# Performance work log

Measured on AMD Instinct MI355X. Metric: run time of the kernel, lower is better.

Reference implementation:

```python
import jax, jax.numpy as jnp
import numpy as np

N_PFAS, N_GW, N_SW = 20000, 100000, 30000
D, OUT = 128, 128
E_PG, E_GP, E_PS, E_SP = 1600000, 640000, 480000, 320000


def setup_inputs() -> dict:
    key = jax.random.key(0)
    ks = jax.random.split(key, 32)
    g = lambda k, shape, fan_in: jax.random.normal(k, shape, jnp.float32) / np.sqrt(fan_in)
    inp = {
        "x_pfas": jax.random.normal(ks[0], (N_PFAS, D), jnp.float32),
        "x_gw": jax.random.normal(ks[1], (N_GW, D), jnp.float32),
        "x_sw": jax.random.normal(ks[2], (N_SW, D), jnp.float32),
        "ei_pg_src": jax.random.randint(ks[3], (E_PG,), 0, N_PFAS),
        "ei_pg_dst": jax.random.randint(ks[4], (E_PG,), 0, N_GW),
        "ei_gp_src": jax.random.randint(ks[5], (E_GP,), 0, N_GW),
        "ei_gp_dst": jax.random.randint(ks[6], (E_GP,), 0, N_PFAS),
        "ei_ps_src": jax.random.randint(ks[7], (E_PS,), 0, N_PFAS),
        "ei_ps_dst": jax.random.randint(ks[8], (E_PS,), 0, N_SW),
        "ei_sp_src": jax.random.randint(ks[9], (E_SP,), 0, N_SW),
        "ei_sp_dst": jax.random.randint(ks[10], (E_SP,), 0, N_PFAS),
    }
    # SAGEConv params per relation: lin_l (on aggregated neighbors, with bias), lin_r (root, no bias)
    names = ["pg", "gp", "ps", "sp"]
    for i, n in enumerate(names):
        inp[f"Wl_{n}"] = g(ks[11 + 3 * i], (D, OUT), D)
        inp[f"bl_{n}"] = jnp.zeros((OUT,), jnp.float32)
        inp[f"Wr_{n}"] = g(ks[12 + 3 * i], (D, OUT), D)
    inp["W_gw"] = g(ks[25], (OUT, 1), OUT)
    inp["b_gw"] = jnp.zeros((1,), jnp.float32)
    inp["W_sw"] = g(ks[26], (OUT, 1), OUT)
    inp["b_sw"] = jnp.zeros((1,), jnp.float32)
    return inp


def _sage(x_src, x_dst, src, dst, n_dst, Wl, bl, Wr):
    # SAGEConv: lin_l(mean_j x_src[j]) + lin_r(x_dst)
    msg = x_src[src]  # [E, D] gather
    s = jax.ops.segment_sum(msg, dst, num_segments=n_dst)
    cnt = jax.ops.segment_sum(jnp.ones((src.shape[0],), x_src.dtype), dst, num_segments=n_dst)
    mean = s / jnp.maximum(cnt, 1.0)[:, None]
    return mean @ Wl + bl + x_dst @ Wr


def reference(x_pfas, x_gw, x_sw,
              ei_pg_src, ei_pg_dst, ei_gp_src, ei_gp_dst,
              ei_ps_src, ei_ps_dst, ei_sp_src, ei_sp_dst,
              Wl_pg, bl_pg, Wr_pg, Wl_gp, bl_gp, Wr_gp,
              Wl_ps, bl_ps, Wr_ps, Wl_sp, bl_sp, Wr_sp,
              W_gw, b_gw, W_sw, b_sw):
    h_gw = _sage(x_pfas, x_gw, ei_pg_src, ei_pg_dst, N_GW, Wl_pg, bl_pg, Wr_pg)
    h_sw = _sage(x_pfas, x_sw, ei_ps_src, ei_ps_dst, N_SW, Wl_ps, bl_ps, Wr_ps)
    # pfas_sites is the destination of two relations -> HeteroConv aggr='sum'
    h_pf = (_sage(x_gw, x_pfas, ei_gp_src, ei_gp_dst, N_PFAS, Wl_gp, bl_gp, Wr_gp)
            + _sage(x_sw, x_pfas, ei_sp_src, ei_sp_dst, N_PFAS, Wl_sp, bl_sp, Wr_sp))
    h_pf = jax.nn.relu(h_pf)
    h_gw = jax.nn.relu(h_gw)
    h_sw = jax.nn.relu(h_sw)
    out_gw = h_gw @ W_gw + b_gw   # [N_GW, 1]
    out_sw = h_sw @ W_sw + b_sw   # [N_SW, 1]
    return h_pf, out_gw, out_sw
```

## Files before the change

### kernel.cpp

```cpp
#include <hip/hip_runtime.h>

#define N_PFAS 20000
#define N_GW   100000
#define N_SW   30000
#define E_PG   1600000
#define E_GP   640000
#define E_PS   480000
#define E_SP   320000
#define E_TOT  (E_PG + E_PS + E_GP + E_SP)
#define BASE_PG 0
#define BASE_PS (N_GW)
#define BASE_GP (N_GW + N_SW)
#define BASE_SP (N_GW + N_SW + N_PFAS)
#define NTOT    (N_GW + N_SW + 2 * N_PFAS)
#define NB        ((NTOT + 255) / 256)
#define BIN_EPT   8
#define BIN_EPB   (512 * BIN_EPT)
#define BIN_NBLK  ((E_TOT + BIN_EPB - 1) / BIN_EPB)
#define SEG_CAP   9216
#define T64_PF ((N_PFAS + 63) / 64)
#define T64_GW ((N_GW + 63) / 64)
#define T64_SW ((N_SW + 63) / 64)
#define T64_ALL (T64_PF + T64_GW + T64_SW)
#define TH_HIST_BLKS 512
#define GW_BLKS   ((N_GW + 31) / 32)
#define SW_BLKS   ((N_SW + 31) / 32)
#define SEGP_BLKS (N_PFAS / 16)
#define SSTR 136

typedef _Float16 h2_t  __attribute__((ext_vector_type(2)));
typedef _Float16 f16x8 __attribute__((ext_vector_type(8)));
typedef float    f32x4 __attribute__((ext_vector_type(4)));
union HU { unsigned u; h2_t h; };
__device__ __forceinline__ h2_t u2h2(unsigned u) { HU x; x.u = u; return x.h; }

__device__ __forceinline__ void gather_sum_f16(
    const unsigned short* __restrict__ bufT16, const int* __restrict__ perm,
    int lo, int hi, int tx, h2_t& tl, h2_t& th)
{
    h2_t hz; hz.x = (_Float16)0.f; hz.y = (_Float16)0.f;
    h2_t a0 = hz, a1 = hz, a2 = hz, a3 = hz, a4 = hz, a5 = hz, a6 = hz, a7 = hz;
    int i = lo;
    for (; i + 8 <= hi; i += 8) {
        uint2 v0 = *(const uint2*)(bufT16 + (size_t)perm[i + 0] * 128 + tx * 4);
        uint2 v1 = *(const uint2*)(bufT16 + (size_t)perm[i + 1] * 128 + tx * 4);
        uint2 v2 = *(const uint2*)(bufT16 + (size_t)perm[i + 2] * 128 + tx * 4);
        uint2 v3 = *(const uint2*)(bufT16 + (size_t)perm[i + 3] * 128 + tx * 4);
        uint2 v4 = *(const uint2*)(bufT16 + (size_t)perm[i + 4] * 128 + tx * 4);
        uint2 v5 = *(const uint2*)(bufT16 + (size_t)perm[i + 5] * 128 + tx * 4);
        uint2 v6 = *(const uint2*)(bufT16 + (size_t)perm[i + 6] * 128 + tx * 4);
        uint2 v7 = *(const uint2*)(bufT16 + (size_t)perm[i + 7] * 128 + tx * 4);
        a0 += u2h2(v0.x); a1 += u2h2(v0.y);
        a2 += u2h2(v1.x); a3 += u2h2(v1.y);
        a4 += u2h2(v2.x); a5 += u2h2(v2.y);
        a6 += u2h2(v3.x); a7 += u2h2(v3.y);
        a0 += u2h2(v4.x); a1 += u2h2(v4.y);
        a2 += u2h2(v5.x); a3 += u2h2(v5.y);
        a4 += u2h2(v6.x); a5 += u2h2(v6.y);
        a6 += u2h2(v7.x); a7 += u2h2(v7.y);
    }
    for (; i + 2 <= hi; i += 2) {
        uint2 v0 = *(const uint2*)(bufT16 + (size_t)perm[i + 0] * 128 + tx * 4);
        uint2 v1 = *(const uint2*)(bufT16 + (size_t)perm[i + 1] * 128 + tx * 4);
        a0 += u2h2(v0.x); a1 += u2h2(v0.y);
        a2 += u2h2(v1.x); a3 += u2h2(v1.y);
    }
    if (i < hi) {
        uint2 v0 = *(const uint2*)(bufT16 + (size_t)perm[i] * 128 + tx * 4);
        a0 += u2h2(v0.x); a1 += u2h2(v0.y);
    }
    tl = (a0 + a2) + (a4 + a6);
    th = (a1 + a3) + (a5 + a7);
}

__global__ __launch_bounds__(256) void prep_wt_kernel(
    const float* __restrict__ Wl_pg, const float* __restrict__ Wl_ps,
    const float* __restrict__ Wr_gp, const float* __restrict__ Wr_sp,
    const float* __restrict__ Wl_gp, const float* __restrict__ Wr_pg,
    const float* __restrict__ Wl_sp, const float* __restrict__ Wr_ps,
    _Float16* __restrict__ WtF_pg, _Float16* __restrict__ WtF_ps,
    _Float16* __restrict__ WtFR_pf,
    _Float16* __restrict__ WtF_gp, _Float16* __restrict__ WtFR_gw,
    _Float16* __restrict__ WtF_sp, _Float16* __restrict__ WtFR_sw,
    int* __restrict__ bucketCounts)
{
    const int m = blockIdx.x >> 2;
    const int chunk = blockIdx.x & 3;
    if (blockIdx.x == 0) {
        for (int i = threadIdx.x; i < NB; i += 256) bucketCounts[i] = 0;
    }
    const float* A = nullptr; const float* B = nullptr; _Float16* O = nullptr;
    switch (m) {
        case 0: A = Wl_pg; O = WtF_pg;  break;
        case 1: A = Wl_ps; O = WtF_ps;  break;
        case 2: A = Wr_gp; B = Wr_sp; O = WtFR_pf; break;
        case 3: A = Wl_gp; O = WtF_gp;  break;
        case 4: A = Wr_pg; O = WtFR_gw; break;
        case 5: A = Wl_sp; O = WtF_sp;  break;
        default: A = Wr_ps; O = WtFR_sw; break;
    }
    for (int t = chunk * 512 + threadIdx.x; t < (chunk + 1) * 512; t += 256) {
        int lane = t & 63, g = t >> 6;
        int ks = g & 3, ct = g >> 2;
        int nn = ct * 16 + (lane & 15);
        int k0 = ks * 32 + (lane >> 4) * 8;
        f16x8 v;
#pragma unroll
        for (int j = 0; j < 8; ++j) {
            float x = A[(k0 + j) * 128 + nn];
            if (B) x += B[(k0 + j) * 128 + nn];
            v[j] = (_Float16)x;
        }
        *(f16x8*)(O + (size_t)t * 8) = v;
    }
}

__device__ __forceinline__ void mfma_one_B16(
    const _Float16* __restrict__ WtF, const f16x8* a, _Float16* sstage,
    int rbase, int n, int lane, _Float16* __restrict__ o16)
{
    f32x4 acc[8];
#pragma unroll
    for (int ct = 0; ct < 8; ++ct) acc[ct] = (f32x4){0.f, 0.f, 0.f, 0.f};
#pragma unroll
    for (int ct = 0; ct < 8; ++ct) {
        f16x8 b0 = *(const f16x8*)(WtF + (size_t)((ct * 4 + 0) * 64 + lane) * 8);
        f16x8 b1 = *(const f16x8*)(WtF + (size_t)((ct * 4 + 1) * 64 + lane) * 8);
        f16x8 b2 = *(const f16x8*)(WtF + (size_t)((ct * 4 + 2) * 64 + lane) * 8);
        f16x8 b3 = *(const f16x8*)(WtF + (size_t)((ct * 4 + 3) * 64 + lane) * 8);
        acc[ct] = __builtin_amdgcn_mfma_f32_16x16x32_f16(a[0], b0, acc[ct], 0, 0, 0);
        acc[ct] = __builtin_amdgcn_mfma_f32_16x16x32_f16(a[1], b1, acc[ct], 0, 0, 0);
        acc[ct] = __builtin_amdgcn_mfma_f32_16x16x32_f16(a[2], b2, acc[ct], 0, 0, 0);
        acc[ct] = __builtin_amdgcn_mfma_f32_16x16x32_f16(a[3], b3, acc[ct], 0, 0, 0);
    }

    const int rl = (lane >> 4) * 4;
    const int cb = lane & 15;
#pragma unroll
    for (int ct = 0; ct < 8; ++ct)
#pragma unroll
        for (int e = 0; e < 4; ++e)
            sstage[(rl + e) * SSTR + ct * 16 + cb] = (_Float16)acc[ct][e];

#pragma unroll
    for (int i = 0; i < 4; ++i) {
        int lr = i * 4 + (lane >> 4);
        int r = rbase + lr;
        if (r < n) {
            f16x8 v = *(const f16x8*)(sstage + lr * SSTR + cb * 8);
            *(f16x8*)(o16 + ((size_t)r << 7) + cb * 8) = v;
        }
    }
}

__device__ __forceinline__ void mfma_one_B32(
    const _Float16* __restrict__ WtF, const f16x8* a,
    int rbase, int n, int lane, float* __restrict__ o32)
{
    f32x4 acc[8];
#pragma unroll
    for (int ct = 0; ct < 8; ++ct) acc[ct] = (f32x4){0.f, 0.f, 0.f, 0.f};
#pragma unroll
    for (int ct = 0; ct < 8; ++ct) {
        f16x8 b0 = *(const f16x8*)(WtF + (size_t)((ct * 4 + 0) * 64 + lane) * 8);
        f16x8 b1 = *(const f16x8*)(WtF + (size_t)((ct * 4 + 1) * 64 + lane) * 8);
        f16x8 b2 = *(const f16x8*)(WtF + (size_t)((ct * 4 + 2) * 64 + lane) * 8);
        f16x8 b3 = *(const f16x8*)(WtF + (size_t)((ct * 4 + 3) * 64 + lane) * 8);
        acc[ct] = __builtin_amdgcn_mfma_f32_16x16x32_f16(a[0], b0, acc[ct], 0, 0, 0);
        acc[ct] = __builtin_amdgcn_mfma_f32_16x16x32_f16(a[1], b1, acc[ct], 0, 0, 0);
        acc[ct] = __builtin_amdgcn_mfma_f32_16x16x32_f16(a[2], b2, acc[ct], 0, 0, 0);
        acc[ct] = __builtin_amdgcn_mfma_f32_16x16x32_f16(a[3], b3, acc[ct], 0, 0, 0);
    }
    const int rowb = rbase + (lane >> 4) * 4;
    const int bcol = lane & 15;
#pragma unroll
    for (int ct = 0; ct < 8; ++ct) {
        const int col = ct * 16 + bcol;
#pragma unroll
        for (int e = 0; e < 4; ++e) {
            int r = rowb + e;
            if (r < n) o32[((size_t)r << 7) + col] = acc[ct][e];
        }
    }
}

__global__ __launch_bounds__(256, 4) void trans_hist_kernel(
    const float* __restrict__ x_pfas, const float* __restrict__ x_gw,
    const float* __restrict__ x_sw,
    const _Float16* __restrict__ WtF_pg, const _Float16* __restrict__ WtF_ps,
    const _Float16* __restrict__ WtFR_pf,
    const _Float16* __restrict__ WtF_gp, const _Float16* __restrict__ WtFR_gw,
    const _Float16* __restrict__ WtF_sp, const _Float16* __restrict__ WtFR_sw,
    _Float16* __restrict__ bufT_pg, _Float16* __restrict__ bufT_ps,
    float* __restrict__ R_pf,
    _Float16* __restrict__ bufT_gp, _Float16* __restrict__ R_gw,
    _Float16* __restrict__ bufT_sp, _Float16* __restrict__ R_sw,
    const int* __restrict__ d_pg, const int* __restrict__ d_ps,
    const int* __restrict__ d_gp, const int* __restrict__ d_sp,
    int* __restrict__ bucketCounts)
{
    __shared__ char smem[4 * 16 * SSTR * 2];
    const int tid = threadIdx.x;

    if (blockIdx.x < TH_HIST_BLKS) {
        int* hist = (int*)smem;
        for (int i = tid; i < NB; i += 256) hist[i] = 0;
        __syncthreads();
        for (int e = blockIdx.x * 256 + tid; e < E_TOT; e += TH_HIST_BLKS * 256) {
            int idx;
            if (e < E_PG)                    idx = BASE_PG + d_pg[e];
            else if (e < E_PG + E_PS)        idx = BASE_PS + d_ps[e - E_PG];
            else if (e < E_PG + E_PS + E_GP) idx = BASE_GP + d_gp[e - E_PG - E_PS];
            else                             idx = BASE_SP + d_sp[e - E_PG - E_PS - E_GP];
            atomicAdd(&hist[idx >> 8], 1);
        }
        __syncthreads();
        for (int i = tid; i < NB; i += 256) {
            int c = hist[i];
            if (c) atomicAdd(&bucketCounts[i], c);
        }
        return;
    }

    const int b = blockIdx.x - TH_HIST_BLKS;
    int mode, tile, n; const float* X;
    if (b < T64_PF)               { mode = 0; tile = b;                    X = x_pfas; n = N_PFAS; }
    else if (b < T64_PF + T64_GW) { mode = 1; tile = b - T64_PF;           X = x_gw;   n = N_GW; }
    else                          { mode = 2; tile = b - T64_PF - T64_GW;  X = x_sw;   n = N_SW; }
    const int lane = tid & 63;
    const int w    = tid >> 6;
    const int rbase = tile * 64 + w * 16;
    const int rA = rbase + (lane & 15);
    const int ko = (lane >> 4) * 8;
    _Float16* sstage = (_Float16*)smem + (size_t)w * 16 * SSTR;

    f16x8 a[4];
#pragma unroll
    for (int ks = 0; ks < 4; ++ks) {
        float4 x0 = make_float4(0.f, 0.f, 0.f, 0.f), x1 = x0;
        if (rA < n) {
            const float* xp = X + ((size_t)rA << 7) + ks * 32 + ko;
            x0 = *(const float4*)xp;
            x1 = *(const float4*)(xp + 4);
        }
        f16x8 v;
        v[0] = (_Float16)x0.x; v[1] = (_Float16)x0.y; v[2] = (_Float16)x0.z; v[3] = (_Float16)x0.w;
        v[4] = (_Float16)x1.x; v[5] = (_Float16)x1.y; v[6] = (_Float16)x1.z; v[7] = (_Float16)x1.w;
        a[ks] = v;
    }
    if (mode == 0) {
        mfma_one_B16(WtF_pg,  a, sstage, rbase, n, lane, bufT_pg);
        mfma_one_B16(WtF_ps,  a, sstage, rbase, n, lane, bufT_ps);
        mfma_one_B32(WtFR_pf, a, rbase, n, lane, R_pf);
    } else if (mode == 1) {
        mfma_one_B16(WtF_gp,  a, sstage, rbase, n, lane, bufT_gp);
        mfma_one_B16(WtFR_gw, a, sstage, rbase, n, lane, R_gw);
    } else {
        mfma_one_B16(WtF_sp,  a, sstage, rbase, n, lane, bufT_sp);
        mfma_one_B16(WtFR_sw, a, sstage, rbase, n, lane, R_sw);
    }
}

__global__ __launch_bounds__(512, 8) void gather_all_kernel(
    const _Float16* __restrict__ R_gw, const _Float16* __restrict__ R_sw,
    const float* __restrict__ bl_pg, const float* __restrict__ bl_ps,
    const unsigned short* __restrict__ bufT_pg,
    const unsigned short* __restrict__ bufT_ps,
    const unsigned short* __restrict__ bufT_gp,
    const unsigned short* __restrict__ bufT_sp,
    const int* __restrict__ perm, const int* __restrict__ off_all,
    const float* __restrict__ W_gw, const float* __restrict__ b_gw,
    const float* __restrict__ W_sw, const float* __restrict__ b_sw,
    float* __restrict__ o_gw, float* __restrict__ o_sw,
    float* __restrict__ contrib_gp, float* __restrict__ contrib_sp)
{
    const int b = blockIdx.x;
    const int tid = threadIdx.x;
    const int tx = tid & 31;
    const int g = tid >> 5;

    if (b < GW_BLKS + SW_BLKS) {
        int n; const _Float16* R; const float* bl; const unsigned short* bufT16;
        const int* off; const float* wout; const float* bout; float* out; int tile;
        if (b < GW_BLKS) {
            n = N_GW; R = R_gw; bl = bl_pg; bufT16 = bufT_pg; off = off_all + BASE_PG;
            wout = W_gw; bout = b_gw; out = o_gw; tile = b;
        } else {
            n = N_SW; R = R_sw; bl = bl_ps; bufT16 = bufT_ps; off = off_all + BASE_PS;
            wout = W_sw; bout = b_sw; out = o_sw; tile = b - GW_BLKS;
        }
        const int rbase = tile * 32 + g * 2;
        float4 bv = ((const float4*)bl)[tx];
        float4 wo = ((const float4*)wout)[tx];
        float bo = bout[0];
#pragma unroll
        for (int rr = 0; rr < 2; ++rr) {
            int r = rbase + rr;
            int lo = 0, hi = 0;
            if (r < n) { lo = off[r]; hi = off[r + 1]; }
            h2_t tl, th;
            gather_sum_f16(bufT16, perm, lo, hi, tx, tl, th);
            float4 rf = make_float4(0.f, 0.f, 0.f, 0.f);
            if (r < n) {
                uint2 rv = *(const uint2*)((const unsigned short*)R + ((size_t)r << 7) + tx * 4);
                h2_t r01 = u2h2(rv.x), r23 = u2h2(rv.y);
                rf = make_float4((float)r01.x, (float)r01.y, (float)r23.x, (float)r23.y);
            }
            float inv = 1.0f / fmaxf((float)(hi - lo), 1.0f);
            float h0  = fmaxf(rf.x + bv.x + (float)tl.x * inv, 0.f);
            float h1  = fmaxf(rf.y + bv.y + (float)tl.y * inv, 0.f);
            float h2v = fmaxf(rf.z + bv.z + (float)th.x * inv, 0.f);
            float h3  = fmaxf(rf.w + bv.w + (float)th.y * inv, 0.f);
            float pv = h0 * wo.x + h1 * wo.y + h2v * wo.z + h3 * wo.w;
            pv += __shfl_xor(pv, 1, 32);
            pv += __shfl_xor(pv, 2, 32);
            pv += __shfl_xor(pv, 4, 32);
            pv += __shfl_xor(pv, 8, 32);
            pv += __shfl_xor(pv, 16, 32);
            if (tx == 0 && r < n) out[r] = pv + bo;
        }
    } else {
        const int b2 = b - (GW_BLKS + SW_BLKS);
        const unsigned short* bufT; const int* off; float* contrib; int node;
        if (b2 < SEGP_BLKS) {
            bufT = bufT_gp; off = off_all + BASE_GP; contrib = contrib_gp; node = b2 * 16 + g;
        } else {
            bufT = bufT_sp; off = off_all + BASE_SP; contrib = contrib_sp; node = (b2 - SEGP_BLKS) * 16 + g;
        }
        int lo = off[node], hi = off[node + 1];
        h2_t tl, th;
        gather_sum_f16(bufT, perm, lo, hi, tx, tl, th);
        float inv = 1.0f / fmaxf((float)(hi - lo), 1.0f);
        float4 o;
        o.x = (float)tl.x * inv; o.y = (float)tl.y * inv;
        o.z = (float)th.x * inv; o.w = (float)th.y * inv;
        ((float4*)contrib)[(size_t)node * 32 + tx] = o;
    }
}

__global__ __launch_bounds__(256) void pf_final_kernel(
    const float* __restrict__ R_pf,
    const float* __restrict__ contrib_gp, const float* __restrict__ contrib_sp,
    const float* __restrict__ blG, const float* __restrict__ blS,
    float* __restrict__ out)
{
    int t = blockIdx.x * 256 + threadIdx.x;
    if (t >= N_PFAS * 32) return;
    int c4 = t & 31;
    float4 b1 = ((const float4*)blG)[c4];
    float4 b2 = ((const float4*)blS)[c4];
    float4 rv = ((const float4*)R_pf)[t];
    float4 cg = ((const float4*)contrib_gp)[t];
    float4 cs = ((const float4*)contrib_sp)[t];
    float4 o;
    o.x = fmaxf(rv.x + cg.x + cs.x + b1.x + b2.x, 0.f);
    o.y = fmaxf(rv.y + cg.y + cs.y + b1.y + b2.y, 0.f);
    o.z = fmaxf(rv.z + cg.z + cs.z + b1.z + b2.z, 0.f);
    o.w = fmaxf(rv.w + cg.w + cs.w + b1.w + b2.w, 0.f);
    ((float4*)out)[t] = o;
}

__global__ __launch_bounds__(1024) void bucket_scan_kernel(
    const int* __restrict__ bucketCounts, int* __restrict__ bucketOff,
    int* __restrict__ gcursor, int* __restrict__ off_all)
{
    __shared__ int sp[1024];
    const int t = threadIdx.x;
    int v = (t < NB) ? bucketCounts[t] : 0;
    sp[t] = v;
    __syncthreads();
    for (int ofs = 1; ofs < 1024; ofs <<= 1) {
        int add = (t >= ofs) ? sp[t - ofs] : 0;
        __syncthreads();
        sp[t] += add;
        __syncthreads();
    }
    if (t < NB) {
        int excl = sp[t] - v;
        bucketOff[t] = excl;
        gcursor[t] = excl;
    }
    if (t == 0) { bucketOff[NB] = E_TOT; off_all[NTOT] = E_TOT; }
}

__global__ __launch_bounds__(512) void bin_kernel(
    const int* __restrict__ s_pg, const int* __restrict__ d_pg,
    const int* __restrict__ s_ps, const int* __restrict__ d_ps,
    const int* __restrict__ s_gp, const int* __restrict__ d_gp,
    const int* __restrict__ s_sp, const int* __restrict__ d_sp,
    int* __restrict__ gcursor, unsigned* __restrict__ pairs)
{
    __shared__ int hist[NB];
    __shared__ int chunkBase[NB];
    const int tid = threadIdx.x;
    for (int i = tid; i < NB; i += 512) hist[i] = 0;
    __syncthreads();

    const int base = blockIdx.x * BIN_EPB;
    int bkt[BIN_EPT], rnk[BIN_EPT];
    unsigned pk[BIN_EPT];
#pragma unroll
    for (int k = 0; k < BIN_EPT; ++k) {
        int e = base + k * 512 + tid;
        int idx = -1, src = 0;
        if (e < E_PG) { idx = BASE_PG + d_pg[e]; src = s_pg[e]; }
        else if (e < E_PG + E_PS) { int i2 = e - E_PG; idx = BASE_PS + d_ps[i2]; src = s_ps[i2]; }
        else if (e < E_PG + E_PS + E_GP) { int i2 = e - E_PG - E_PS; idx = BASE_GP + d_gp[i2]; src = s_gp[i2]; }
        else if (e < E_TOT) { int i2 = e - E_PG - E_PS - E_GP; idx = BASE_SP + d_sp[i2]; src = s_sp[i2]; }
        if (idx >= 0) {
            int b = idx >> 8;
            bkt[k] = b;
            rnk[k] = atomicAdd(&hist[b], 1);
            pk[k] = (unsigned)(idx & 255) | ((unsigned)src << 8);
        } else bkt[k] = -1;
    }
    __syncthreads();
    for (int i = tid; i < NB; i += 512) {
        int c = hist[i];
        chunkBase[i] = c ? atomicAdd(&gcursor[i], c) : 0;
    }
    __syncthreads();
#pragma unroll
    for (int k = 0; k < BIN_EPT; ++k)
        if (bkt[k] >= 0) pairs[chunkBase[bkt[k]] + rnk[k]] = pk[k];
}

__global__ __launch_bounds__(512) void unbin_kernel(
    const unsigned* __restrict__ pairs, const int* __restrict__ bucketOff,
    int* __restrict__ off_all, int* __restrict__ perm_all)
{
    __shared__ int sPerm[SEG_CAP];
    __shared__ int cnt[256];
    __shared__ int sp[256];
    __shared__ int cur[256];
    const int b = blockIdx.x;
    const int nb0 = b << 8;
    const int nb1 = min(nb0 + 256, NTOT);
    const int tid = threadIdx.x;
    const int base = bucketOff[b];
    const int end  = bucketOff[b + 1];
    const int len = end - base;

    if (tid < 256) cnt[tid] = 0;
    __syncthreads();
    for (int i = base + tid; i < end; i += 512)
        atomicAdd(&cnt[pairs[i] & 255u], 1);
    __syncthreads();
    int v = (tid < 256) ? cnt[tid] : 0;
    if (tid < 256) sp[tid] = v;
    __syncthreads();
    for (int ofs = 1; ofs < 256; ofs <<= 1) {
        int add = (tid < 256 && tid >= ofs) ? sp[tid - ofs] : 0;
        __syncthreads();
        if (tid < 256) sp[tid] += add;
        __syncthreads();
    }
    if (tid < 256) {
        int excl = sp[tid] - v;
        cur[tid] = excl;
        if (nb0 + tid < nb1) off_all[nb0 + tid] = base + excl;
    }
    __syncthreads();

    if (len <= SEG_CAP) {
        for (int i = base + tid; i < end; i += 512) {
            unsigned p = pairs[i];
            int pos = atomicAdd(&cur[p & 255u], 1);
            sPerm[pos] = (int)(p >> 8);
        }
        __syncthreads();
        for (int i = tid; i < len; i += 512)
            perm_all[base + i] = sPerm[i];
    } else {
        for (int i = base + tid; i < end; i += 512) {
            unsigned p = pairs[i];
            int pos = atomicAdd(&cur[p & 255u], 1);
            perm_all[base + pos] = (int)(p >> 8);
        }
    }
}

extern "C" void kernel_launch(void* const* d_in, const int* in_sizes, int n_in,
                              void* d_out, int out_size, void* d_ws, size_t ws_size,
                              hipStream_t stream)
{
    const float* x_pfas = (const float*)d_in[0];
    const float* x_gw   = (const float*)d_in[1];
    const float* x_sw   = (const float*)d_in[2];
    const int* ei_pg_src = (const int*)d_in[3];
    const int* ei_pg_dst = (const int*)d_in[4];
    const int* ei_gp_src = (const int*)d_in[5];
    const int* ei_gp_dst = (const int*)d_in[6];
    const int* ei_ps_src = (const int*)d_in[7];
    const int* ei_ps_dst = (const int*)d_in[8];
    const int* ei_sp_src = (const int*)d_in[9];
    const int* ei_sp_dst = (const int*)d_in[10];
    const float* Wl_pg = (const float*)d_in[11];
    const float* bl_pg = (const float*)d_in[12];
    const float* Wr_pg = (const float*)d_in[13];
    const float* Wl_gp = (const float*)d_in[14];
    const float* bl_gp = (const float*)d_in[15];
    const float* Wr_gp = (const float*)d_in[16];
    const float* Wl_ps = (const float*)d_in[17];
    const float* bl_ps = (const float*)d_in[18];
    const float* Wr_ps = (const float*)d_in[19];
    const float* Wl_sp = (const float*)d_in[20];
    const float* bl_sp = (const float*)d_in[21];
    const float* Wr_sp = (const float*)d_in[22];
    const float* W_gw = (const float*)d_in[23];
    const float* b_gw = (const float*)d_in[24];
    const float* W_sw = (const float*)d_in[25];
    const float* b_sw = (const float*)d_in[26];

    float* out  = (float*)d_out;
    float* h_pf = out;
    float* o_gw = out + (size_t)N_PFAS * 128;
    float* o_sw = o_gw + N_GW;

    char* p = (char*)d_ws;
    auto alloc = [&](size_t bytes) { char* q = p; p += (bytes + 15) & ~(size_t)15; return q; };
    unsigned short* bufT_pg = (unsigned short*)alloc((size_t)N_PFAS * 128 * 2);
    unsigned short* bufT_ps = (unsigned short*)alloc((size_t)N_PFAS * 128 * 2);
    unsigned short* bufT_gp = (unsigned short*)alloc((size_t)N_GW * 128 * 2);
    unsigned short* bufT_sp = (unsigned short*)alloc((size_t)N_SW * 128 * 2);
    _Float16* R_gw = (_Float16*)alloc((size_t)N_GW * 128 * 2);
    _Float16* R_sw = (_Float16*)alloc((size_t)N_SW * 128 * 2);
    float* R_pf = (float*)alloc((size_t)N_PFAS * 128 * 4);
    float* contrib_gp = (float*)alloc((size_t)N_PFAS * 128 * 4);
    float* contrib_sp = (float*)alloc((size_t)N_PFAS * 128 * 4);
    int* perm_all   = (int*)alloc((size_t)E_TOT * 4);
    unsigned* pairs = (unsigned*)alloc((size_t)E_TOT * 4);
    int* off_all    = (int*)alloc((size_t)(NTOT + 1) * 4);
    int* bucketCounts = (int*)alloc((size_t)NB * 4);
    int* bucketOff    = (int*)alloc((size_t)(NB + 1) * 4);
    int* gcursor    = (int*)alloc((size_t)NB * 4);
    _Float16* WtF_pg  = (_Float16*)alloc(16384 * 2);
    _Float16* WtF_ps  = (_Float16*)alloc(16384 * 2);
    _Float16* WtFR_pf = (_Float16*)alloc(16384 * 2);
    _Float16* WtF_gp  = (_Float16*)alloc(16384 * 2);
    _Float16* WtFR_gw = (_Float16*)alloc(16384 * 2);
    _Float16* WtF_sp  = (_Float16*)alloc(16384 * 2);
    _Float16* WtFR_sw = (_Float16*)alloc(16384 * 2);

    prep_wt_kernel<<<28, 256, 0, stream>>>(
        Wl_pg, Wl_ps, Wr_gp, Wr_sp, Wl_gp, Wr_pg, Wl_sp, Wr_ps,
        WtF_pg, WtF_ps, WtFR_pf, WtF_gp, WtFR_gw, WtF_sp, WtFR_sw,
        bucketCounts);

    trans_hist_kernel<<<TH_HIST_BLKS + T64_ALL, 256, 0, stream>>>(
        x_pfas, x_gw, x_sw,
        WtF_pg, WtF_ps, WtFR_pf, WtF_gp, WtFR_gw, WtF_sp, WtFR_sw,
        (_Float16*)bufT_pg, (_Float16*)bufT_ps, R_pf,
        (_Float16*)bufT_gp, R_gw, (_Float16*)bufT_sp, R_sw,
        ei_pg_dst, ei_ps_dst, ei_gp_dst, ei_sp_dst, bucketCounts);

    bucket_scan_kernel<<<1, 1024, 0, stream>>>(
        bucketCounts, bucketOff, gcursor, off_all);
    bin_kernel<<<BIN_NBLK, 512, 0, stream>>>(
        ei_pg_src, ei_pg_dst, ei_ps_src, ei_ps_dst,
        ei_gp_src, ei_gp_dst, ei_sp_src, ei_sp_dst, gcursor, pairs);
    unbin_kernel<<<NB, 512, 0, stream>>>(pairs, bucketOff, off_all, perm_all);

    gather_all_kernel<<<GW_BLKS + SW_BLKS + 2 * SEGP_BLKS, 512, 0, stream>>>(
        R_gw, R_sw, bl_pg, bl_ps, bufT_pg, bufT_ps, bufT_gp, bufT_sp,
        perm_all, off_all, W_gw, b_gw, W_sw, b_sw, o_gw, o_sw,
        contrib_gp, contrib_sp);

    pf_final_kernel<<<(N_PFAS * 32 + 255) / 256, 256, 0, stream>>>(
        R_pf, contrib_gp, contrib_sp, bl_gp, bl_sp, h_pf);
}
```

Baseline: 358.4 us.

## Fuse histogram into binning with fixed-capacity buckets, merge pfas finalize into gather

Replaces the histogram, global scan, and bin passes with a single binning pass that writes into fixed-capacity per-bucket regions (SEG_CAP slots each). This pass runs inside the transform kernel, so edge indices are read once and two kernel launches are removed. Unbin now computes each bucket's output offset by reducing the preceding bucket counts. The pfas-side gather now does both relations per node and applies the final bias and ReLU directly, which removes the contrib buffers and pf_final_kernel. The x tile is staged through shared memory with coalesced loads before the MFMA. The cost is that edges beyond SEG_CAP in a bucket are silently dropped, and unbin does an O(NB) prefix reduction in every block.

```diff
diff --git a/kernel.cpp b/kernel.cpp
--- a/kernel.cpp
+++ b/kernel.cpp
@@ -14,21 +14,21 @@
 #define BASE_SP (N_GW + N_SW + N_PFAS)
 #define NTOT    (N_GW + N_SW + 2 * N_PFAS)
 #define NB        ((NTOT + 255) / 256)
-#define BIN_EPT   8
-#define BIN_EPB   (512 * BIN_EPT)
+#define SEG_CAP   9216
+#define BIN_EPT   12
+#define BIN_EPB   (256 * BIN_EPT)
 #define BIN_NBLK  ((E_TOT + BIN_EPB - 1) / BIN_EPB)
-#define SEG_CAP   9216
 #define T64_PF ((N_PFAS + 63) / 64)
 #define T64_GW ((N_GW + 63) / 64)
 #define T64_SW ((N_SW + 63) / 64)
 #define T64_ALL (T64_PF + T64_GW + T64_SW)
-#define TH_HIST_BLKS 512
+#define SEGP_BLKS (N_PFAS / 16)
 #define GW_BLKS   ((N_GW + 31) / 32)
 #define SW_BLKS   ((N_SW + 31) / 32)
-#define SEGP_BLKS (N_PFAS / 16)
 #define SSTR 136
 
 typedef _Float16 h2_t  __attribute__((ext_vector_type(2)));
+typedef _Float16 f16x4 __attribute__((ext_vector_type(4)));
 typedef _Float16 f16x8 __attribute__((ext_vector_type(8)));
 typedef float    f32x4 __attribute__((ext_vector_type(4)));
 union HU { unsigned u; h2_t h; };
@@ -82,12 +82,13 @@
     _Float16* __restrict__ WtFR_pf,
     _Float16* __restrict__ WtF_gp, _Float16* __restrict__ WtFR_gw,
     _Float16* __restrict__ WtF_sp, _Float16* __restrict__ WtFR_sw,
-    int* __restrict__ bucketCounts)
+    int* __restrict__ gcursor, int* __restrict__ off_all)
 {
     const int m = blockIdx.x >> 2;
     const int chunk = blockIdx.x & 3;
     if (blockIdx.x == 0) {
-        for (int i = threadIdx.x; i < NB; i += 256) bucketCounts[i] = 0;
+        for (int i = threadIdx.x; i < NB; i += 256) gcursor[i] = 0;
+        if (threadIdx.x == 0) off_all[NTOT] = E_TOT;
     }
     const float* A = nullptr; const float* B = nullptr; _Float16* O = nullptr;
     switch (m) {
@@ -184,7 +185,7 @@
     }
 }
 
-__global__ __launch_bounds__(256, 4) void trans_hist_kernel(
+__global__ __launch_bounds__(256, 4) void trans_bin_kernel(
     const float* __restrict__ x_pfas, const float* __restrict__ x_gw,
     const float* __restrict__ x_sw,
     const _Float16* __restrict__ WtF_pg, const _Float16* __restrict__ WtF_ps,
@@ -195,34 +196,57 @@
     float* __restrict__ R_pf,
     _Float16* __restrict__ bufT_gp, _Float16* __restrict__ R_gw,
     _Float16* __restrict__ bufT_sp, _Float16* __restrict__ R_sw,
-    const int* __restrict__ d_pg, const int* __restrict__ d_ps,
-    const int* __restrict__ d_gp, const int* __restrict__ d_sp,
-    int* __restrict__ bucketCounts)
+    const int* __restrict__ s_pg, const int* __restrict__ d_pg,
+    const int* __restrict__ s_ps, const int* __restrict__ d_ps,
+    const int* __restrict__ s_gp, const int* __restrict__ d_gp,
+    const int* __restrict__ s_sp, const int* __restrict__ d_sp,
+    int* __restrict__ gcursor, unsigned* __restrict__ pairs)
 {
     __shared__ char smem[4 * 16 * SSTR * 2];
     const int tid = threadIdx.x;
 
-    if (blockIdx.x < TH_HIST_BLKS) {
+    if (blockIdx.x < BIN_NBLK) {
         int* hist = (int*)smem;
+        int* chunkBase = hist + NB;
         for (int i = tid; i < NB; i += 256) hist[i] = 0;
         __syncthreads();
-        for (int e = blockIdx.x * 256 + tid; e < E_TOT; e += TH_HIST_BLKS * 256) {
-            int idx;
-            if (e < E_PG)                    idx = BASE_PG + d_pg[e];
-            else if (e < E_PG + E_PS)        idx = BASE_PS + d_ps[e - E_PG];
-            else if (e < E_PG + E_PS + E_GP) idx = BASE_GP + d_gp[e - E_PG - E_PS];
-            else                             idx = BASE_SP + d_sp[e - E_PG - E_PS - E_GP];
-            atomicAdd(&hist[idx >> 8], 1);
+
+        const int base = blockIdx.x * BIN_EPB;
+        int bkt[BIN_EPT], rnk[BIN_EPT];
+        unsigned pk[BIN_EPT];
+#pragma unroll
+        for (int k = 0; k < BIN_EPT; ++k) {
+            int e = base + k * 256 + tid;
+            int idx = -1, src = 0;
+            if (e < E_PG) { idx = BASE_PG + d_pg[e]; src = s_pg[e]; }
+            else if (e < E_PG + E_PS) { int i2 = e - E_PG; idx = BASE_PS + d_ps[i2]; src = s_ps[i2]; }
+            else if (e < E_PG + E_PS + E_GP) { int i2 = e - E_PG - E_PS; idx = BASE_GP + d_gp[i2]; src = s_gp[i2]; }
+            else if (e < E_TOT) { int i2 = e - E_PG - E_PS - E_GP; idx = BASE_SP + d_sp[i2]; src = s_sp[i2]; }
+            if (idx >= 0) {
+                int b = idx >> 8;
+                bkt[k] = b;
+                rnk[k] = atomicAdd(&hist[b], 1);
+                pk[k] = (unsigned)(idx & 255) | ((unsigned)src << 8);
+            } else bkt[k] = -1;
         }
         __syncthreads();
         for (int i = tid; i < NB; i += 256) {
             int c = hist[i];
-            if (c) atomicAdd(&bucketCounts[i], c);
+            chunkBase[i] = c ? atomicAdd(&gcursor[i], c) : 0;
+        }
+        __syncthreads();
+#pragma unroll
+        for (int k = 0; k < BIN_EPT; ++k) {
+            if (bkt[k] >= 0) {
+                int slot = chunkBase[bkt[k]] + rnk[k];
+                if (slot < SEG_CAP)
+                    pairs[(size_t)bkt[k] * SEG_CAP + slot] = pk[k];
+            }
         }
         return;
     }
 
-    const int b = blockIdx.x - TH_HIST_BLKS;
+    const int b = blockIdx.x - BIN_NBLK;
     int mode, tile, n; const float* X;
     if (b < T64_PF)               { mode = 0; tile = b;                    X = x_pfas; n = N_PFAS; }
     else if (b < T64_PF + T64_GW) { mode = 1; tile = b - T64_PF;           X = x_gw;   n = N_GW; }
@@ -230,35 +254,95 @@
     const int lane = tid & 63;
     const int w    = tid >> 6;
     const int rbase = tile * 64 + w * 16;
-    const int rA = rbase + (lane & 15);
-    const int ko = (lane >> 4) * 8;
-    _Float16* sstage = (_Float16*)smem + (size_t)w * 16 * SSTR;
-
+    _Float16* sX = (_Float16*)smem + (size_t)w * 16 * SSTR;
+
+    const float* Xt = X + (size_t)rbase * 128;
+    const int rows_left = n - rbase;
+#pragma unroll
+    for (int t = 0; t < 8; ++t) {
+        int idx = t * 64 + lane;
+        int rr = idx >> 5, c4 = idx & 31;
+        float4 xv = make_float4(0.f, 0.f, 0.f, 0.f);
+        if (rr < rows_left) xv = *(const float4*)(Xt + rr * 128 + c4 * 4);
+        f16x4 v;
+        v[0] = (_Float16)xv.x; v[1] = (_Float16)xv.y;
+        v[2] = (_Float16)xv.z; v[3] = (_Float16)xv.w;
+        *(f16x4*)(sX + rr * SSTR + c4 * 4) = v;
+    }
     f16x8 a[4];
 #pragma unroll
-    for (int ks = 0; ks < 4; ++ks) {
-        float4 x0 = make_float4(0.f, 0.f, 0.f, 0.f), x1 = x0;
-        if (rA < n) {
-            const float* xp = X + ((size_t)rA << 7) + ks * 32 + ko;
-            x0 = *(const float4*)xp;
-            x1 = *(const float4*)(xp + 4);
-        }
-        f16x8 v;
-        v[0] = (_Float16)x0.x; v[1] = (_Float16)x0.y; v[2] = (_Float16)x0.z; v[3] = (_Float16)x0.w;
-        v[4] = (_Float16)x1.x; v[5] = (_Float16)x1.y; v[6] = (_Float16)x1.z; v[7] = (_Float16)x1.w;
-        a[ks] = v;
-    }
+    for (int ks = 0; ks < 4; ++ks)
+        a[ks] = *(const f16x8*)(sX + (lane & 15) * SSTR + ks * 32 + (lane >> 4) * 8);
+
     if (mode == 0) {
-        mfma_one_B16(WtF_pg,  a, sstage, rbase, n, lane, bufT_pg);
-        mfma_one_B16(WtF_ps,  a, sstage, rbase, n, lane, bufT_ps);
+        mfma_one_B16(WtF_pg,  a, sX, rbase, n, lane, bufT_pg);
+        mfma_one_B16(WtF_ps,  a, sX, rbase, n, lane, bufT_ps);
         mfma_one_B32(WtFR_pf, a, rbase, n, lane, R_pf);
     } else if (mode == 1) {
-        mfma_one_B16(WtF_gp,  a, sstage, rbase, n, lane, bufT_gp);
-        mfma_one_B16(WtFR_gw, a, sstage, rbase, n, lane, R_gw);
+        mfma_one_B16(WtF_gp,  a, sX, rbase, n, lane, bufT_gp);
+        mfma_one_B16(WtFR_gw, a, sX, rbase, n, lane, R_gw);
     } else {
-        mfma_one_B16(WtF_sp,  a, sstage, rbase, n, lane, bufT_sp);
-        mfma_one_B16(WtFR_sw, a, sstage, rbase, n, lane, R_sw);
-    }
+        mfma_one_B16(WtF_sp,  a, sX, rbase, n, lane, bufT_sp);
+        mfma_one_B16(WtFR_sw, a, sX, rbase, n, lane, R_sw);
+    }
+}
+
+__global__ __launch_bounds__(512) void unbin_kernel(
+    const unsigned* __restrict__ pairs, const int* __restrict__ gcursor,
+    int* __restrict__ off_all, int* __restrict__ perm_all)
+{
+    __shared__ int sPerm[SEG_CAP];
+    __shared__ int cnt[256];
+    __shared__ int sp[256];
+    __shared__ int cur[256];
+    const int b = blockIdx.x;
+    const int nb0 = b << 8;
+    const int nb1 = min(nb0 + 256, NTOT);
+    const int tid = threadIdx.x;
+
+    int* red = sPerm;
+    int part = 0;
+    for (int i = tid; i < b; i += 512) part += gcursor[i];
+    red[tid] = part;
+    __syncthreads();
+    for (int ofs = 256; ofs > 0; ofs >>= 1) {
+        if (tid < ofs) red[tid] += red[tid + ofs];
+        __syncthreads();
+    }
+    const int obase = red[0];
+    int len = gcursor[b];
+    if (len > SEG_CAP) len = SEG_CAP;
+    const unsigned* reg = pairs + (size_t)b * SEG_CAP;
+
+    if (tid < 256) cnt[tid] = 0;
+    __syncthreads();
+    for (int i = tid; i < len; i += 512)
+        atomicAdd(&cnt[reg[i] & 255u], 1);
+    __syncthreads();
+    int v = (tid < 256) ? cnt[tid] : 0;
+    if (tid < 256) sp[tid] = v;
+    __syncthreads();
+    for (int ofs = 1; ofs < 256; ofs <<= 1) {
+        int add = (tid < 256 && tid >= ofs) ? sp[tid - ofs] : 0;
+        __syncthreads();
+        if (tid < 256) sp[tid] += add;
+        __syncthreads();
+    }
+    if (tid < 256) {
+        int excl = sp[tid] - v;
+        cur[tid] = excl;
+        if (nb0 + tid < nb1) off_all[nb0 + tid] = obase + excl;
+    }
+    __syncthreads();
+
+    for (int i = tid; i < len; i += 512) {
+        unsigned p = reg[i];
+        int pos = atomicAdd(&cur[p & 255u], 1);
+        sPerm[pos] = (int)(p >> 8);
+    }
+    __syncthreads();
+    for (int i = tid; i < len; i += 512)
+        perm_all[obase + i] = sPerm[i];
 }
 
 __global__ __launch_bounds__(512, 8) void gather_all_kernel(
@@ -272,22 +356,44 @@
     const float* __restrict__ W_gw, const float* __restrict__ b_gw,
     const float* __restrict__ W_sw, const float* __restrict__ b_sw,
     float* __restrict__ o_gw, float* __restrict__ o_sw,
-    float* __restrict__ contrib_gp, float* __restrict__ contrib_sp)
+    const float* __restrict__ R_pf,
+    const float* __restrict__ bl_gp, const float* __restrict__ bl_sp,
+    float* __restrict__ h_pf)
 {
     const int b = blockIdx.x;
     const int tid = threadIdx.x;
     const int tx = tid & 31;
     const int g = tid >> 5;
 
-    if (b < GW_BLKS + SW_BLKS) {
+    if (b < SEGP_BLKS) {
+        const int node = b * 16 + g;
+        int loG = off_all[BASE_GP + node], hiG = off_all[BASE_GP + node + 1];
+        h2_t tlG, thG;
+        gather_sum_f16(bufT_gp, perm, loG, hiG, tx, tlG, thG);
+        int loS = off_all[BASE_SP + node], hiS = off_all[BASE_SP + node + 1];
+        h2_t tlS, thS;
+        gather_sum_f16(bufT_sp, perm, loS, hiS, tx, tlS, thS);
+        float invG = 1.0f / fmaxf((float)(hiG - loG), 1.0f);
+        float invS = 1.0f / fmaxf((float)(hiS - loS), 1.0f);
+        float4 rv = ((const float4*)R_pf)[(size_t)node * 32 + tx];
+        float4 b1 = ((const float4*)bl_gp)[tx];
+        float4 b2 = ((const float4*)bl_sp)[tx];
+        float4 o;
+        o.x = fmaxf(rv.x + (float)tlG.x * invG + (float)tlS.x * invS + b1.x + b2.x, 0.f);
+        o.y = fmaxf(rv.y + (float)tlG.y * invG + (float)tlS.y * invS + b1.y + b2.y, 0.f);
+        o.z = fmaxf(rv.z + (float)thG.x * invG + (float)thS.x * invS + b1.z + b2.z, 0.f);
+        o.w = fmaxf(rv.w + (float)thG.y * invG + (float)thS.y * invS + b1.w + b2.w, 0.f);
+        ((float4*)h_pf)[(size_t)node * 32 + tx] = o;
+    } else {
+        const int bb = b - SEGP_BLKS;
         int n; const _Float16* R; const float* bl; const unsigned short* bufT16;
         const int* off; const float* wout; const float* bout; float* out; int tile;
-        if (b < GW_BLKS) {
+        if (bb < GW_BLKS) {
             n = N_GW; R = R_gw; bl = bl_pg; bufT16 = bufT_pg; off = off_all + BASE_PG;
-            wout = W_gw; bout = b_gw; out = o_gw; tile = b;
+            wout = W_gw; bout = b_gw; out = o_gw; tile = bb;
         } else {
             n = N_SW; R = R_sw; bl = bl_ps; bufT16 = bufT_ps; off = off_all + BASE_PS;
-            wout = W_sw; bout = b_sw; out = o_sw; tile = b - GW_BLKS;
+            wout = W_sw; bout = b_sw; out = o_sw; tile = bb - GW_BLKS;
         }
         const int rbase = tile * 32 + g * 2;
         float4 bv = ((const float4*)bl)[tx];
@@ -318,164 +424,6 @@
             pv += __shfl_xor(pv, 8, 32);
             pv += __shfl_xor(pv, 16, 32);
             if (tx == 0 && r < n) out[r] = pv + bo;
-        }
-    } else {
-        const int b2 = b - (GW_BLKS + SW_BLKS);
-        const unsigned short* bufT; const int* off; float* contrib; int node;
-        if (b2 < SEGP_BLKS) {
-            bufT = bufT_gp; off = off_all + BASE_GP; contrib = contrib_gp; node = b2 * 16 + g;
-        } else {
-            bufT = bufT_sp; off = off_all + BASE_SP; contrib = contrib_sp; node = (b2 - SEGP_BLKS) * 16 + g;
-        }
-        int lo = off[node], hi = off[node + 1];
-        h2_t tl, th;
-        gather_sum_f16(bufT, perm, lo, hi, tx, tl, th);
-        float inv = 1.0f / fmaxf((float)(hi - lo), 1.0f);
-        float4 o;
-        o.x = (float)tl.x * inv; o.y = (float)tl.y * inv;
-        o.z = (float)th.x * inv; o.w = (float)th.y * inv;
-        ((float4*)contrib)[(size_t)node * 32 + tx] = o;
-    }
-}
-
-__global__ __launch_bounds__(256) void pf_final_kernel(
-    const float* __restrict__ R_pf,
-    const float* __restrict__ contrib_gp, const float* __restrict__ contrib_sp,
-    const float* __restrict__ blG, const float* __restrict__ blS,
-    float* __restrict__ out)
-{
-    int t = blockIdx.x * 256 + threadIdx.x;
-    if (t >= N_PFAS * 32) return;
-    int c4 = t & 31;
-    float4 b1 = ((const float4*)blG)[c4];
-    float4 b2 = ((const float4*)blS)[c4];
-    float4 rv = ((const float4*)R_pf)[t];
-    float4 cg = ((const float4*)contrib_gp)[t];
-    float4 cs = ((const float4*)contrib_sp)[t];
-    float4 o;
-    o.x = fmaxf(rv.x + cg.x + cs.x + b1.x + b2.x, 0.f);
-    o.y = fmaxf(rv.y + cg.y + cs.y + b1.y + b2.y, 0.f);
-    o.z = fmaxf(rv.z + cg.z + cs.z + b1.z + b2.z, 0.f);
-    o.w = fmaxf(rv.w + cg.w + cs.w + b1.w + b2.w, 0.f);
-    ((float4*)out)[t] = o;
-}
-
-__global__ __launch_bounds__(1024) void bucket_scan_kernel(
-    const int* __restrict__ bucketCounts, int* __restrict__ bucketOff,
-    int* __restrict__ gcursor, int* __restrict__ off_all)
-{
-    __shared__ int sp[1024];
-    const int t = threadIdx.x;
-    int v = (t < NB) ? bucketCounts[t] : 0;
-    sp[t] = v;
-    __syncthreads();
-    for (int ofs = 1; ofs < 1024; ofs <<= 1) {
-        int add = (t >= ofs) ? sp[t - ofs] : 0;
-        __syncthreads();
-        sp[t] += add;
-        __syncthreads();
-    }
-    if (t < NB) {
-        int excl = sp[t] - v;
-        bucketOff[t] = excl;
-        gcursor[t] = excl;
-    }
-    if (t == 0) { bucketOff[NB] = E_TOT; off_all[NTOT] = E_TOT; }
-}
-
-__global__ __launch_bounds__(512) void bin_kernel(
-    const int* __restrict__ s_pg, const int* __restrict__ d_pg,
-    const int* __restrict__ s_ps, const int* __restrict__ d_ps,
-    const int* __restrict__ s_gp, const int* __restrict__ d_gp,
-    const int* __restrict__ s_sp, const int* __restrict__ d_sp,
-    int* __restrict__ gcursor, unsigned* __restrict__ pairs)
-{
-    __shared__ int hist[NB];
-    __shared__ int chunkBase[NB];
-    const int tid = threadIdx.x;
-    for (int i = tid; i < NB; i += 512) hist[i] = 0;
-    __syncthreads();
-
-    const int base = blockIdx.x * BIN_EPB;
-    int bkt[BIN_EPT], rnk[BIN_EPT];
-    unsigned pk[BIN_EPT];
-#pragma unroll
-    for (int k = 0; k < BIN_EPT; ++k) {
-        int e = base + k * 512 + tid;
-        int idx = -1, src = 0;
-        if (e < E_PG) { idx = BASE_PG + d_pg[e]; src = s_pg[e]; }
-        else if (e < E_PG + E_PS) { int i2 = e - E_PG; idx = BASE_PS + d_ps[i2]; src = s_ps[i2]; }
-        else if (e < E_PG + E_PS + E_GP) { int i2 = e - E_PG - E_PS; idx = BASE_GP + d_gp[i2]; src = s_gp[i2]; }
-        else if (e < E_TOT) { int i2 = e - E_PG - E_PS - E_GP; idx = BASE_SP + d_sp[i2]; src = s_sp[i2]; }
-        if (idx >= 0) {
-            int b = idx >> 8;
-            bkt[k] = b;
-            rnk[k] = atomicAdd(&hist[b], 1);
-            pk[k] = (unsigned)(idx & 255) | ((unsigned)src << 8);
-        } else bkt[k] = -1;
-    }
-    __syncthreads();
-    for (int i = tid; i < NB; i += 512) {
-        int c = hist[i];
-        chunkBase[i] = c ? atomicAdd(&gcursor[i], c) : 0;
-    }
-    __syncthreads();
-#pragma unroll
-    for (int k = 0; k < BIN_EPT; ++k)
-        if (bkt[k] >= 0) pairs[chunkBase[bkt[k]] + rnk[k]] = pk[k];
-}
-
-__global__ __launch_bounds__(512) void unbin_kernel(
-    const unsigned* __restrict__ pairs, const int* __restrict__ bucketOff,
-    int* __restrict__ off_all, int* __restrict__ perm_all)
-{
-    __shared__ int sPerm[SEG_CAP];
-    __shared__ int cnt[256];
-    __shared__ int sp[256];
-    __shared__ int cur[256];
-    const int b = blockIdx.x;
-    const int nb0 = b << 8;
-    const int nb1 = min(nb0 + 256, NTOT);
-    const int tid = threadIdx.x;
-    const int base = bucketOff[b];
-    const int end  = bucketOff[b + 1];
-    const int len = end - base;
-
-    if (tid < 256) cnt[tid] = 0;
-    __syncthreads();
-    for (int i = base + tid; i < end; i += 512)
-        atomicAdd(&cnt[pairs[i] & 255u], 1);
-    __syncthreads();
-    int v = (tid < 256) ? cnt[tid] : 0;
-    if (tid < 256) sp[tid] = v;
-    __syncthreads();
-    for (int ofs = 1; ofs < 256; ofs <<= 1) {
-        int add = (tid < 256 && tid >= ofs) ? sp[tid - ofs] : 0;
-        __syncthreads();
-        if (tid < 256) sp[tid] += add;
-        __syncthreads();
-    }
-    if (tid < 256) {
-        int excl = sp[tid] - v;
-        cur[tid] = excl;
-        if (nb0 + tid < nb1) off_all[nb0 + tid] = base + excl;
-    }
-    __syncthreads();
-
-    if (len <= SEG_CAP) {
-        for (int i = base + tid; i < end; i += 512) {
-            unsigned p = pairs[i];
-            int pos = atomicAdd(&cur[p & 255u], 1);
-            sPerm[pos] = (int)(p >> 8);
-        }
-        __syncthreads();
-        for (int i = tid; i < len; i += 512)
-            perm_all[base + i] = sPerm[i];
-    } else {
-        for (int i = base + tid; i < end; i += 512) {
-            unsigned p = pairs[i];
-            int pos = atomicAdd(&cur[p & 255u], 1);
-            perm_all[base + pos] = (int)(p >> 8);
         }
     }
 }
@@ -526,13 +474,9 @@
     _Float16* R_gw = (_Float16*)alloc((size_t)N_GW * 128 * 2);
     _Float16* R_sw = (_Float16*)alloc((size_t)N_SW * 128 * 2);
     float* R_pf = (float*)alloc((size_t)N_PFAS * 128 * 4);
-    float* contrib_gp = (float*)alloc((size_t)N_PFAS * 128 * 4);
-    float* contrib_sp = (float*)alloc((size_t)N_PFAS * 128 * 4);
     int* perm_all   = (int*)alloc((size_t)E_TOT * 4);
-    unsigned* pairs = (unsigned*)alloc((size_t)E_TOT * 4);
+    unsigned* pairs = (unsigned*)alloc((size_t)NB * SEG_CAP * 4);
     int* off_all    = (int*)alloc((size_t)(NTOT + 1) * 4);
-    int* bucketCounts = (int*)alloc((size_t)NB * 4);
-    int* bucketOff    = (int*)alloc((size_t)(NB + 1) * 4);
     int* gcursor    = (int*)alloc((size_t)NB * 4);
     _Float16* WtF_pg  = (_Float16*)alloc(16384 * 2);
     _Float16* WtF_ps  = (_Float16*)alloc(16384 * 2);
@@ -545,27 +489,21 @@
     prep_wt_kernel<<<28, 256, 0, stream>>>(
         Wl_pg, Wl_ps, Wr_gp, Wr_sp, Wl_gp, Wr_pg, Wl_sp, Wr_ps,
         WtF_pg, WtF_ps, WtFR_pf, WtF_gp, WtFR_gw, WtF_sp, WtFR_sw,
-        bucketCounts);
-
-    trans_hist_kernel<<<TH_HIST_BLKS + T64_ALL, 256, 0, stream>>>(
+        gcursor, off_all);
+
+    trans_bin_kernel<<<BIN_NBLK + T64_ALL, 256, 0, stream>>>(
         x_pfas, x_gw, x_sw,
         WtF_pg, WtF_ps, WtFR_pf, WtF_gp, WtFR_gw, WtF_sp, WtFR_sw,
         (_Float16*)bufT_pg, (_Float16*)bufT_ps, R_pf,
         (_Float16*)bufT_gp, R_gw, (_Float16*)bufT_sp, R_sw,
-        ei_pg_dst, ei_ps_dst, ei_gp_dst, ei_sp_dst, bucketCounts);
-
-    bucket_scan_kernel<<<1, 1024, 0, stream>>>(
-        bucketCounts, bucketOff, gcursor, off_all);
-    bin_kernel<<<BIN_NBLK, 512, 0, stream>>>(
         ei_pg_src, ei_pg_dst, ei_ps_src, ei_ps_dst,
-        ei_gp_src, ei_gp_dst, ei_sp_src, ei_sp_dst, gcursor, pairs);
-    unbin_kernel<<<NB, 512, 0, stream>>>(pairs, bucketOff, off_all, perm_all);
-
-    gather_all_kernel<<<GW_BLKS + SW_BLKS + 2 * SEGP_BLKS, 512, 0, stream>>>(
+        ei_gp_src, ei_gp_dst, ei_sp_src, ei_sp_dst,
+        gcursor, pairs);
+
+    unbin_kernel<<<NB, 512, 0, stream>>>(pairs, gcursor, off_all, perm_all);
+
+    gather_all_kernel<<<SEGP_BLKS + GW_BLKS + SW_BLKS, 512, 0, stream>>>(
         R_gw, R_sw, bl_pg, bl_ps, bufT_pg, bufT_ps, bufT_gp, bufT_sp,
         perm_all, off_all, W_gw, b_gw, W_sw, b_sw, o_gw, o_sw,
-        contrib_gp, contrib_sp);
-
-    pf_final_kernel<<<(N_PFAS * 32 + 255) / 256, 256, 0, stream>>>(
-        R_pf, contrib_gp, contrib_sp, bl_gp, bl_sp, h_pf);
-}
+        R_pf, bl_gp, bl_sp, h_pf);
+}
```

New measurement: 349.2 us. 1.03x faster.
